# Kernel optimization log

Measured on AMD Instinct MI355X. Metric: run time of the kernel, lower is better.

Reference implementation:

```python
import jax, jax.numpy as jnp
import numpy as np

EPS = 1e-10  # faithful to original: masked scores are set to eps, not -inf


def setup_inputs() -> dict:
    key = jax.random.key(0)
    ks = jax.random.split(key, 5)
    B, S, D, N, H = 2, 2048, 1024, 16, 64
    init_range = 0.02
    residual = jax.random.normal(ks[0], (B, S, D), dtype=jnp.float32)
    W_key = jax.random.normal(ks[1], (N, D, H), dtype=jnp.float32) * init_range
    W_query = jax.random.normal(ks[2], (N, D, H), dtype=jnp.float32) * init_range
    W_values = jax.random.normal(ks[3], (N, D, H), dtype=jnp.float32) * init_range
    W_output = jax.random.normal(ks[4], (N, H, D), dtype=jnp.float32) * init_range
    return {
        "residual": residual,
        "W_key": W_key, "W_query": W_query, "W_values": W_values, "W_output": W_output,
        "Bias_key": jnp.zeros((N, H), jnp.float32),
        "Bias_query": jnp.zeros((N, H), jnp.float32),
        "Bias_values": jnp.zeros((N, H), jnp.float32),
        "Bias_output": jnp.zeros((D,), jnp.float32),
    }


def reference(residual, W_key, W_query, W_values, W_output,
              Bias_key, Bias_query, Bias_values, Bias_output):
    B, S, D = residual.shape
    N, _, H = W_key.shape
    # projections: [b,s,n,h]
    keys = jnp.einsum('bse,neh->bsnh', residual, W_key) + Bias_key
    queries = jnp.einsum('bse,neh->bsnh', residual, W_query) + Bias_query
    values = jnp.einsum('bse,neh->bsnh', residual, W_values) + Bias_values
    # scores: [b,n,q,k]
    scores = jnp.einsum('bknh,bqnh->bnqk', keys, queries) / jnp.sqrt(jnp.asarray(H, scores_dtype(residual)))
    q_idx = jnp.arange(S)[:, None]
    k_idx = jnp.arange(S)[None, :]
    causal_mask = q_idx < k_idx  # future positions
    # QUIRK of original module: masked scores are assigned eps (~0), not -inf
    scores = jnp.where(causal_mask[None, None, :, :], jnp.asarray(EPS, scores.dtype), scores)
    probs = jax.nn.softmax(scores, axis=3)
    weighted = jnp.einsum('bnqk,bknh->bqnh', probs, values)
    out = jnp.einsum('bqnh,nhe->bqe', weighted, W_output) + Bias_output
    return out


def scores_dtype(x):
    return x.dtype
```

## Files before the change

kernel.cpp:

```cpp
#include <hip/hip_runtime.h>
#include <hip/hip_bf16.h>
#include <cmath>

typedef __bf16 bf16;
typedef __attribute__((ext_vector_type(4))) __bf16 bf16x4;
typedef __attribute__((ext_vector_type(8))) __bf16 bf16x8;
typedef __attribute__((ext_vector_type(4))) float f32x4;

#define B_ 2
#define S_ 2048
#define D_ 1024
#define N_ 16
#define H_ 64
#define LOG2E 1.44269504088896340736f

__device__ __forceinline__ void gload16(const bf16* g, bf16* l) {
  __builtin_amdgcn_global_load_lds(
      (const __attribute__((address_space(1))) void*)(g),
      (__attribute__((address_space(3))) void*)(l), 16, 0, 0);
}

__device__ __forceinline__ f32x4 mfma16(bf16x8 a, bf16x8 b, f32x4 c) {
  return __builtin_amdgcn_mfma_f32_16x16x32_bf16(a, b, c, 0, 0, 0);
}

__device__ __forceinline__ f32x4 zero4() {
  f32x4 v = {0.0f, 0.0f, 0.0f, 0.0f};
  return v;
}

__global__ __launch_bounds__(256) void cvt_kernel(
    const float* __restrict__ in, bf16* __restrict__ out, int n8) {
  int id = blockIdx.x * 256 + threadIdx.x;
  if (id >= n8) return;
  const float4* p = (const float4*)(in + (size_t)id * 8);
  float4 v0 = p[0], v1 = p[1];
  bf16x8 o;
  o[0] = (bf16)v0.x; o[1] = (bf16)v0.y; o[2] = (bf16)v0.z; o[3] = (bf16)v0.w;
  o[4] = (bf16)v1.x; o[5] = (bf16)v1.y; o[6] = (bf16)v1.z; o[7] = (bf16)v1.w;
  *(bf16x8*)(out + (size_t)id * 8) = o;
}

__global__ __launch_bounds__(256) void qkvw_transpose_kernel(
    const float* __restrict__ Wk, const float* __restrict__ Wq,
    const float* __restrict__ Wv, bf16* __restrict__ out) {
  __shared__ bf16 t[64][72];
  const int z = blockIdx.z;
  const float* W = (z < 16) ? Wk : (z < 32) ? Wq : Wv;
  const float* ing = W + (size_t)(z & 15) * (1024 * 64);
  bf16* outg = out + (size_t)z * (64 * 1024);
  const int r0 = blockIdx.x * 64;
  const int t8 = threadIdx.x & 7, trow = threadIdx.x >> 3;
#pragma unroll
  for (int p = 0; p < 2; ++p) {
    int r = trow + p * 32;
    const float4* src = (const float4*)(ing + (size_t)(r0 + r) * 64 + t8 * 8);
    float4 v0 = src[0], v1 = src[1];
    bf16x8 o;
    o[0] = (bf16)v0.x; o[1] = (bf16)v0.y; o[2] = (bf16)v0.z; o[3] = (bf16)v0.w;
    o[4] = (bf16)v1.x; o[5] = (bf16)v1.y; o[6] = (bf16)v1.z; o[7] = (bf16)v1.w;
    *(bf16x8*)(&t[r][t8 * 8]) = o;
  }
  __syncthreads();
#pragma unroll
  for (int p = 0; p < 2; ++p) {
    int c = trow + p * 32;
    bf16x8 v;
#pragma unroll
    for (int j = 0; j < 8; ++j) v[j] = t[t8 * 8 + j][c];
    *(bf16x8*)(outg + (size_t)c * 1024 + r0 + t8 * 8) = v;
  }
}

__global__ __launch_bounds__(256) void transpose_f32bf16_kernel(
    const float* __restrict__ in, bf16* __restrict__ out, int R, int C) {
  __shared__ bf16 t[64][72];
  const size_t mat = (size_t)R * C;
  const float* ing = in + (size_t)blockIdx.z * mat;
  bf16* outg = out + (size_t)blockIdx.z * mat;
  const int r0 = blockIdx.x * 64, c0 = blockIdx.y * 64;
  const int t8 = threadIdx.x & 7, trow = threadIdx.x >> 3;
#pragma unroll
  for (int p = 0; p < 2; ++p) {
    int r = trow + p * 32;
    const float4* src = (const float4*)(ing + (size_t)(r0 + r) * C + c0 + t8 * 8);
    float4 v0 = src[0], v1 = src[1];
    bf16x8 o;
    o[0] = (bf16)v0.x; o[1] = (bf16)v0.y; o[2] = (bf16)v0.z; o[3] = (bf16)v0.w;
    o[4] = (bf16)v1.x; o[5] = (bf16)v1.y; o[6] = (bf16)v1.z; o[7] = (bf16)v1.w;
    *(bf16x8*)(&t[r][t8 * 8]) = o;
  }
  __syncthreads();
#pragma unroll
  for (int p = 0; p < 2; ++p) {
    int c = trow + p * 32;
    bf16x8 v;
#pragma unroll
    for (int j = 0; j < 8; ++j) v[j] = t[t8 * 8 + j][c];
    *(bf16x8*)(outg + (size_t)(c0 + c) * R + r0 + t8 * 8) = v;
  }
}

__global__ __launch_bounds__(256) void transpose_bf16_kernel(
    const bf16* __restrict__ in, bf16* __restrict__ out, int R, int C) {
  __shared__ bf16 t[64][72];
  const size_t mat = (size_t)R * C;
  const bf16* ing = in + (size_t)blockIdx.z * mat;
  bf16* outg = out + (size_t)blockIdx.z * mat;
  const int r0 = blockIdx.x * 64, c0 = blockIdx.y * 64;
  const int t8 = threadIdx.x & 7, trow = threadIdx.x >> 3;
#pragma unroll
  for (int p = 0; p < 2; ++p) {
    int r = trow + p * 32;
    bf16x8 v = *(const bf16x8*)(ing + (size_t)(r0 + r) * C + c0 + t8 * 8);
    *(bf16x8*)(&t[r][t8 * 8]) = v;
  }
  __syncthreads();
#pragma unroll
  for (int p = 0; p < 2; ++p) {
    int c = trow + p * 32;
    bf16x8 v;
#pragma unroll
    for (int j = 0; j < 8; ++j) v[j] = t[t8 * 8 + j][c];
    *(bf16x8*)(outg + (size_t)(c0 + c) * R + r0 + t8 * 8) = v;
  }
}

__global__ __launch_bounds__(256) void sufv_tot_kernel(
    const bf16* __restrict__ Vp, float* __restrict__ tot) {
  __shared__ float red[4][64];
  const int hd = blockIdx.x, seg = blockIdx.y;
  const int h = threadIdx.x & 63, sub = threadIdx.x >> 6;
  const bf16* Vh = Vp + (size_t)hd * S_ * H_;
  float a = 0.0f;
  const int k0 = seg * 32 + sub * 8;
#pragma unroll
  for (int k = 0; k < 8; ++k) a += (float)Vh[(size_t)(k0 + k) * H_ + h];
  red[sub][h] = a;
  __syncthreads();
  if (sub == 0)
    tot[(hd * 64 + seg) * 64 + h] = red[0][h] + red[1][h] + red[2][h] + red[3][h];
}

__global__ __launch_bounds__(64) void sufv_scan_kernel(
    bf16* __restrict__ VS, const float* __restrict__ tot) {
  const int hd = blockIdx.x, seg = blockIdx.y, h = threadIdx.x;
  bf16* Vh = VS + (size_t)hd * S_ * H_;
  float a = 0.0f;
  for (int s2 = seg + 1; s2 < 64; ++s2) a += tot[(hd * 64 + s2) * 64 + h];
  for (int k = seg * 32 + 31; k >= seg * 32; --k) {
    const float v = (float)Vh[(size_t)k * H_ + h];
    Vh[(size_t)k * H_ + h] = (bf16)a;
    a += v;
  }
}

__global__ __launch_bounds__(256) void gemm_proj_kernel(
    const bf16* __restrict__ A, const bf16* __restrict__ Bt,
    const float* __restrict__ bk, const float* __restrict__ bq,
    const float* __restrict__ bv, bf16* __restrict__ proj_base) {
  __shared__ bf16 As[128 * 64];
  __shared__ bf16 Bs[128 * 64];
  const int tid = threadIdx.x;
  const int w = tid >> 6, l = tid & 63, lan = l & 15, grp = l >> 4;
  const int mb = (w >> 1) * 64, nb = (w & 1) * 64;
  const int m0 = blockIdx.y * 128, n0 = blockIdx.x * 128;
  const int zc = n0 >> 10;
  const float* bias = (zc == 0) ? bk : (zc == 1 ? bq : bv);
  bf16* Out = proj_base + (size_t)zc * ((size_t)B_ * N_ * S_ * H_);
  const int lrow8 = l >> 3;
  const int swl = ((l & 7) ^ lrow8) * 8;
  const int l7 = lan & 7;

  f32x4 acc[4][4];
#pragma unroll
  for (int i = 0; i < 4; ++i)
#pragma unroll
    for (int j = 0; j < 4; ++j) acc[i][j] = zero4();

  for (int kb = 0; kb < 1024; kb += 64) {
    __syncthreads();
#pragma unroll
    for (int i = 0; i < 4; ++i) {
      int ch = w * 4 + i;
      gload16(A + (size_t)(m0 + ch * 8 + lrow8) * 1024 + kb + swl, As + ch * 512);
      gload16(Bt + (size_t)(n0 + ch * 8 + lrow8) * 1024 + kb + swl, Bs + ch * 512);
    }
    __syncthreads();
#pragma unroll
    for (int kk = 0; kk < 2; ++kk) {
      bf16x8 a[4], b[4];
#pragma unroll
      for (int mf = 0; mf < 4; ++mf)
        a[mf] = *(const bf16x8*)(As + (mb + mf * 16 + lan) * 64 + (((grp + kk * 4) ^ l7) << 3));
#pragma unroll
      for (int nf = 0; nf < 4; ++nf)
        b[nf] = *(const bf16x8*)(Bs + (nb + nf * 16 + lan) * 64 + (((grp + kk * 4) ^ l7) << 3));
#pragma unroll
      for (int mf = 0; mf < 4; ++mf)
#pragma unroll
        for (int nf = 0; nf < 4; ++nf)
          acc[mf][nf] = mfma16(a[mf], b[nf], acc[mf][nf]);
    }
  }
#pragma unroll
  for (int nf = 0; nf < 4; ++nf) {
    int c10 = (n0 + nb + nf * 16 + lan) & 1023;
    float bs = bias[c10];
    int n = c10 >> 6, h = c10 & 63;
#pragma unroll
    for (int mf = 0; mf < 4; ++mf) {
#pragma unroll
      for (int r = 0; r < 4; ++r) {
        int m = m0 + mb + mf * 16 + grp * 4 + r;
        int b = m >> 11, s = m & 2047;
        Out[((size_t)((b * N_ + n) * S_ + s)) * H_ + h] = (bf16)(acc[mf][nf][r] + bs);
      }
    }
  }
}

__global__ __launch_bounds__(256) void gemm_out_kernel(
    const bf16* __restrict__ A, const bf16* __restrict__ Bt,
    const float* __restrict__ bias, float* __restrict__ Out) {
  __shared__ bf16 As[128 * 64];
  __shared__ bf16 Bs[128 * 64];
  const int tid = threadIdx.x;
  const int w = tid >> 6, l = tid & 63, lan = l & 15, grp = l >> 4;
  const int mb = (w >> 1) * 64, nb = (w & 1) * 64;
  const int m0 = blockIdx.y * 128, n0 = blockIdx.x * 128;
  const int lrow8 = l >> 3;
  const int swl = ((l & 7) ^ lrow8) * 8;
  const int l7 = lan & 7;

  f32x4 acc[4][4];
#pragma unroll
  for (int i = 0; i < 4; ++i)
#pragma unroll
    for (int j = 0; j < 4; ++j) acc[i][j] = zero4();

  for (int kb = 0; kb < 1024; kb += 64) {
    __syncthreads();
#pragma unroll
    for (int i = 0; i < 4; ++i) {
      int ch = w * 4 + i;
      gload16(A + (size_t)(m0 + ch * 8 + lrow8) * 1024 + kb + swl, As + ch * 512);
      gload16(Bt + (size_t)(n0 + ch * 8 + lrow8) * 1024 + kb + swl, Bs + ch * 512);
    }
    __syncthreads();
#pragma unroll
    for (int kk = 0; kk < 2; ++kk) {
      bf16x8 a[4], b[4];
#pragma unroll
      for (int mf = 0; mf < 4; ++mf)
        a[mf] = *(const bf16x8*)(As + (mb + mf * 16 + lan) * 64 + (((grp + kk * 4) ^ l7) << 3));
#pragma unroll
      for (int nf = 0; nf < 4; ++nf)
        b[nf] = *(const bf16x8*)(Bs + (nb + nf * 16 + lan) * 64 + (((grp + kk * 4) ^ l7) << 3));
#pragma unroll
      for (int mf = 0; mf < 4; ++mf)
#pragma unroll
        for (int nf = 0; nf < 4; ++nf)
          acc[mf][nf] = mfma16(a[mf], b[nf], acc[mf][nf]);
    }
  }
#pragma unroll
  for (int nf = 0; nf < 4; ++nf) {
    int c = n0 + nb + nf * 16 + lan;
    float bs = bias[c];
#pragma unroll
    for (int mf = 0; mf < 4; ++mf) {
#pragma unroll
      for (int r = 0; r < 4; ++r) {
        int m = m0 + mb + mf * 16 + grp * 4 + r;
        Out[(size_t)m * 1024 + c] = acc[mf][nf][r] + bs;
      }
    }
  }
}

__global__ __launch_bounds__(256) void attn_kernel(
    const bf16* __restrict__ Qp, const bf16* __restrict__ Kp,
    const bf16* __restrict__ Vt, const bf16* __restrict__ Suf,
    bf16* __restrict__ Wtd, float* __restrict__ PoA, float* __restrict__ PoB,
    float* __restrict__ PpA, float* __restrict__ PpB) {
  __shared__ bf16 Ks[2][64 * 64];
  __shared__ bf16 Vs[2][64 * 64];
  __shared__ bf16 Ps[4][32 * 72];
  const int tid = threadIdx.x;
  const int w = tid >> 6, l = tid & 63, lan = l & 15, grp = l >> 4;
  const int bi = blockIdx.x;
  const int qq = bi >> 8;
  const int j = bi & 255;
  const int hd = j & 31, wv = j >> 5;
  int x, t0, t1;
  if (qq == 0)      { x = 15 - wv; t0 = 0;     t1 = x + 1; }
  else if (qq == 1) { x = 15 - wv; t0 = x + 1; t1 = 2 * x + 2; }
  else              { x = wv;      t0 = 0;     t1 = 2 * x + 2; }
  const int qw = x * 128 + w * 32;
  const bf16* Qh = Qp + (size_t)hd * S_ * H_;
  const bf16* Kh = Kp + (size_t)hd * S_ * H_;
  const bf16* Vh = Vt + (size_t)hd * H_ * S_;
  const bf16* Sufh = Suf + (size_t)hd * S_ * H_;
  const int lrow8 = l >> 3;
  const int swl = ((l & 7) ^ lrow8) * 8;
  const int l7 = lan & 7;
  const float cexp = 0.125f * LOG2E;

#define STAGE(buf, kb_)                                                        \
  do {                                                                         \
    _Pragma("unroll") for (int i2 = 0; i2 < 2; ++i2) {                         \
      int ch = w * 2 + i2;                                                     \
      gload16(Kh + (size_t)((kb_) + ch * 8 + lrow8) * H_ + swl,                \
              &Ks[buf][ch * 512]);                                             \
      gload16(Vh + (size_t)(ch * 8 + lrow8) * S_ + (kb_) + swl,                \
              &Vs[buf][ch * 512]);                                             \
    }                                                                          \
  } while (0)

  bf16x8 qa[2][2];
#pragma unroll
  for (int qt = 0; qt < 2; ++qt)
#pragma unroll
    for (int kf = 0; kf < 2; ++kf)
      qa[qt][kf] = *(const bf16x8*)(Qh + (size_t)(qw + qt * 16 + lan) * H_ + grp * 8 + kf * 32);

  f32x4 o[2][4];
  float psum[2] = {0.0f, 0.0f};
#pragma unroll
  for (int qt = 0; qt < 2; ++qt)
#pragma unroll
    for (int hf = 0; hf < 4; ++hf) o[qt][hf] = zero4();

  bf16* Pw = &Ps[w][0];

  STAGE(0, t0 * 64);
  for (int tt = t0; tt < t1; ++tt) {
    const int kb = tt * 64;
    const int cur = (tt - t0) & 1;
    if (tt + 1 < t1) {
      STAGE(cur ^ 1, kb + 64);
      asm volatile("s_waitcnt vmcnt(4)" ::: "memory");
    } else {
      asm volatile("s_waitcnt vmcnt(0)" ::: "memory");
    }
    __builtin_amdgcn_s_barrier();

    if (kb <= qw + 31) {
      const bf16* Kc = &Ks[cur][0];
      const bf16* Vc = &Vs[cur][0];

      f32x4 s2[4][2];
#pragma unroll
      for (int k2 = 0; k2 < 4; ++k2)
#pragma unroll
        for (int qt = 0; qt < 2; ++qt) s2[k2][qt] = zero4();
      __builtin_amdgcn_s_setprio(1);
#pragma unroll
      for (int kf = 0; kf < 2; ++kf) {
        bf16x8 kfr[4];
#pragma unroll
        for (int k2 = 0; k2 < 4; ++k2)
          kfr[k2] = *(const bf16x8*)(Kc + (k2 * 16 + lan) * 64 + (((grp + kf * 4) ^ l7) << 3));
#pragma unroll
        for (int k2 = 0; k2 < 4; ++k2)
#pragma unroll
          for (int qt = 0; qt < 2; ++qt)
            s2[k2][qt] = mfma16(kfr[k2], qa[qt][kf], s2[k2][qt]);
      }
      __builtin_amdgcn_s_setprio(0);

      const bool maskt = (kb + 63 > qw);
#pragma unroll
      for (int qt = 0; qt < 2; ++qt) {
        const int q_g = qw + qt * 16 + lan;
#pragma unroll
        for (int k2 = 0; k2 < 4; ++k2) {
          f32x4 p;
#pragma unroll
          for (int r = 0; r < 4; ++r) p[r] = exp2f(s2[k2][qt][r] * cexp);
          if (maskt) {
            const int kg0 = kb + k2 * 16 + grp * 4;
#pragma unroll
            for (int r = 0; r < 4; ++r)
              if (kg0 + r > q_g) p[r] = 0.0f;
          }
          psum[qt] += (p[0] + p[1]) + (p[2] + p[3]);
          unsigned plo, phi;
          asm("v_cvt_pk_bf16_f32 %0, %1, %2" : "=v"(plo) : "v"(p[0]), "v"(p[1]));
          asm("v_cvt_pk_bf16_f32 %0, %1, %2" : "=v"(phi) : "v"(p[2]), "v"(p[3]));
          uint2 u; u.x = plo; u.y = phi;
          *(uint2*)(Pw + (qt * 16 + lan) * 72 + k2 * 16 + grp * 4) = u;
        }
      }

      __builtin_amdgcn_s_setprio(1);
#pragma unroll
      for (int ks = 0; ks < 2; ++ks) {
        bf16x8 pa[2], vb[4];
#pragma unroll
        for (int qt = 0; qt < 2; ++qt)
          pa[qt] = *(const bf16x8*)(Pw + (qt * 16 + lan) * 72 + grp * 8 + ks * 32);
#pragma unroll
        for (int hf = 0; hf < 4; ++hf)
          vb[hf] = *(const bf16x8*)(Vc + (hf * 16 + lan) * 64 + (((grp + ks * 4) ^ l7) << 3));
#pragma unroll
        for (int qt = 0; qt < 2; ++qt)
#pragma unroll
          for (int hf = 0; hf < 4; ++hf)
            o[qt][hf] = mfma16(pa[qt], vb[hf], o[qt][hf]);
      }
      __builtin_amdgcn_s_setprio(0);
    }
    __builtin_amdgcn_s_barrier();
  }
#undef STAGE

#pragma unroll
  for (int qt = 0; qt < 2; ++qt) {
    psum[qt] += __shfl_xor(psum[qt], 16);
    psum[qt] += __shfl_xor(psum[qt], 32);
  }

  if (qq == 2) {
    const size_t outbase = (size_t)(hd >> 4) * S_ * (N_ * H_) + (size_t)(hd & 15) * H_;
#pragma unroll
    for (int qt = 0; qt < 2; ++qt) {
#pragma unroll
      for (int r = 0; r < 4; ++r) {
        const int q_g = qw + qt * 16 + grp * 4 + r;
        const float ps = __shfl(psum[qt], grp * 4 + r);
        const float inv = 1.0f / (ps + (float)(2047 - q_g));
#pragma unroll
        for (int hf = 0; hf < 4; ++hf) {
          const int h = hf * 16 + lan;
          const float suf = (float)Sufh[(size_t)q_g * H_ + h];
          Wtd[outbase + (size_t)q_g * (N_ * H_) + h] = (bf16)((o[qt][hf][r] + suf) * inv);
        }
      }
    }
  } else {
    float* Po = (qq == 0) ? PoA : PoB;
    float* Pp = (qq == 0) ? PpA : PpB;
    const int pb = (hd * 8 + (x - 8)) * 128 + w * 32;
#pragma unroll
    for (int qt = 0; qt < 2; ++qt) {
#pragma unroll
      for (int r = 0; r < 4; ++r) {
        const int rl = qt * 16 + grp * 4 + r;
        const float ps = __shfl(psum[qt], grp * 4 + r);
        if (lan == 0) Pp[pb + rl] = ps;
#pragma unroll
        for (int hf = 0; hf < 4; ++hf)
          Po[(size_t)(pb + rl) * 64 + hf * 16 + lan] = o[qt][hf][r];
      }
    }
  }
}

__global__ __launch_bounds__(256) void combine_kernel(
    const float* __restrict__ PoA, const float* __restrict__ PoB,
    const float* __restrict__ PpA, const float* __restrict__ PpB,
    const bf16* __restrict__ Suf, bf16* __restrict__ Wtd) {
  const int hd = blockIdx.x >> 3, xi = blockIdx.x & 7;
  const int x = xi + 8;
  const int pb = (hd * 8 + xi) * 128;
  const size_t outbase = (size_t)(hd >> 4) * S_ * (N_ * H_) + (size_t)(hd & 15) * H_;
#pragma unroll
  for (int it = 0; it < 8; ++it) {
    const int e = it * 256 + threadIdx.x;
    const int rl = e >> 4, h4 = (e & 15) * 4;
    const int q_g = x * 128 + rl;
    const float Z = PpA[pb + rl] + PpB[pb + rl] + (float)(2047 - q_g);
    const float inv = 1.0f / Z;
    const float4 a = *(const float4*)(PoA + (size_t)(pb + rl) * 64 + h4);
    const float4 b = *(const float4*)(PoB + (size_t)(pb + rl) * 64 + h4);
    const bf16x4 s4 = *(const bf16x4*)(Suf + ((size_t)hd * S_ + q_g) * 64 + h4);
    bf16x4 ov;
    ov[0] = (bf16)((a.x + b.x + (float)s4[0]) * inv);
    ov[1] = (bf16)((a.y + b.y + (float)s4[1]) * inv);
    ov[2] = (bf16)((a.z + b.z + (float)s4[2]) * inv);
    ov[3] = (bf16)((a.w + b.w + (float)s4[3]) * inv);
    *(bf16x4*)(Wtd + outbase + (size_t)q_g * (N_ * H_) + h4) = ov;
  }
}

extern "C" void kernel_launch(void* const* d_in, const int* in_sizes, int n_in,
                              void* d_out, int out_size, void* d_ws, size_t ws_size,
                              hipStream_t stream) {
  const float* residual = (const float*)d_in[0];
  const float* Wk = (const float*)d_in[1];
  const float* Wq = (const float*)d_in[2];
  const float* Wv = (const float*)d_in[3];
  const float* Wo = (const float*)d_in[4];
  const float* Bk = (const float*)d_in[5];
  const float* Bq = (const float*)d_in[6];
  const float* Bv = (const float*)d_in[7];
  const float* Bo = (const float*)d_in[8];
  float* outp = (float*)d_out;

  char* ws = (char*)d_ws;
  const size_t MB = 1024 * 1024;
  bf16* Abf = (bf16*)(ws + 0 * MB);
  bf16* Wot = (bf16*)(ws + 8 * MB);
  bf16* Wkt = (bf16*)(ws + 10 * MB);
  bf16* Kp  = (bf16*)(ws + 16 * MB);
  bf16* Qp  = (bf16*)(ws + 24 * MB);
  bf16* Vp  = (bf16*)(ws + 32 * MB);
  bf16* Vtp = (bf16*)(ws + 40 * MB);
  bf16* Wtd = Abf;
  float* PpA = (float*)(ws + 10 * MB);
  float* PpB = (float*)(ws + 10 * MB + 128 * 1024);
  float* tot = (float*)(ws + 10 * MB + 256 * 1024);
  bf16* Suf = Vp;
  float* PoA = (float*)d_out;
  float* PoB = (float*)d_out + 2 * 1024 * 1024;
  (void)in_sizes; (void)n_in; (void)out_size; (void)ws_size;

  cvt_kernel<<<2048, 256, 0, stream>>>(residual, Abf, (B_ * S_ * D_) / 8);

  qkvw_transpose_kernel<<<dim3(16, 1, 48), 256, 0, stream>>>(Wk, Wq, Wv, Wkt);
  transpose_f32bf16_kernel<<<dim3(16, 16, 1), 256, 0, stream>>>(Wo, Wot, 1024, 1024);

  gemm_proj_kernel<<<dim3(24, 32), 256, 0, stream>>>(Abf, Wkt, Bk, Bq, Bv, Kp);

  sufv_tot_kernel<<<dim3(32, 64), 256, 0, stream>>>(Vp, tot);
  transpose_bf16_kernel<<<dim3(32, 1, 32), 256, 0, stream>>>(Vp, Vtp, 2048, 64);
  sufv_scan_kernel<<<dim3(32, 64), 64, 0, stream>>>(Vp, tot);

  attn_kernel<<<768, 256, 0, stream>>>(Qp, Kp, Vtp, Suf, Wtd, PoA, PoB, PpA, PpB);

  combine_kernel<<<256, 256, 0, stream>>>(PoA, PoB, PpA, PpB, Suf, Wtd);

  gemm_out_kernel<<<dim3(8, 32, 1), 256, 0, stream>>>(Wtd, Wot, Bo, outp);
}
```

Baseline: 155.2 us.

## Rewrite QKV projection GEMM with 256x256 tiles and double-buffered LDS pipeline

The QKV projection GEMM moves from 128x128 tiles with 4 waves to 256x256 tiles with 8 waves, each wave computing a 128x64 sub-tile. It double-buffers LDS across K-halves and issues the global-to-LDS loads for the next K step in between MFMA phases, with explicit vmcnt waits and barriers. It also raises MFMA priority via s_setprio. The aim is to overlap memory latency with compute and raise arithmetic intensity, at the cost of more registers and LDS per block and only 192 blocks, which may underfill the GPU's CUs.

New measurement: 149.0 us. -4.0%, faster.

```diff
diff --git a/kernel.cpp b/kernel.cpp
--- a/kernel.cpp
+++ b/kernel.cpp
@@ -155,66 +155,112 @@
   }
 }
 
-__global__ __launch_bounds__(256) void gemm_proj_kernel(
+__global__ __launch_bounds__(512) void gemm_proj_kernel(
     const bf16* __restrict__ A, const bf16* __restrict__ Bt,
     const float* __restrict__ bk, const float* __restrict__ bq,
     const float* __restrict__ bv, bf16* __restrict__ proj_base) {
-  __shared__ bf16 As[128 * 64];
-  __shared__ bf16 Bs[128 * 64];
+  __shared__ bf16 As[2][2][256 * 32];
+  __shared__ bf16 Bs[2][2][256 * 32];
   const int tid = threadIdx.x;
   const int w = tid >> 6, l = tid & 63, lan = l & 15, grp = l >> 4;
-  const int mb = (w >> 1) * 64, nb = (w & 1) * 64;
-  const int m0 = blockIdx.y * 128, n0 = blockIdx.x * 128;
+  const int wm128 = (w >> 2) * 128, wn64 = (w & 3) * 64;
+  const int m0 = blockIdx.y * 256, n0 = blockIdx.x * 256;
   const int zc = n0 >> 10;
   const float* bias = (zc == 0) ? bk : (zc == 1 ? bq : bv);
   bf16* Out = proj_base + (size_t)zc * ((size_t)B_ * N_ * S_ * H_);
-  const int lrow8 = l >> 3;
-  const int swl = ((l & 7) ^ lrow8) * 8;
-  const int l7 = lan & 7;
-
-  f32x4 acc[4][4];
-#pragma unroll
-  for (int i = 0; i < 4; ++i)
-#pragma unroll
-    for (int j = 0; j < 4; ++j) acc[i][j] = zero4();
-
-  for (int kb = 0; kb < 1024; kb += 64) {
-    __syncthreads();
-#pragma unroll
-    for (int i = 0; i < 4; ++i) {
-      int ch = w * 4 + i;
-      gload16(A + (size_t)(m0 + ch * 8 + lrow8) * 1024 + kb + swl, As + ch * 512);
-      gload16(Bt + (size_t)(n0 + ch * 8 + lrow8) * 1024 + kb + swl, Bs + ch * 512);
-    }
-    __syncthreads();
-#pragma unroll
-    for (int kk = 0; kk < 2; ++kk) {
-      bf16x8 a[4], b[4];
-#pragma unroll
-      for (int mf = 0; mf < 4; ++mf)
-        a[mf] = *(const bf16x8*)(As + (mb + mf * 16 + lan) * 64 + (((grp + kk * 4) ^ l7) << 3));
-#pragma unroll
-      for (int nf = 0; nf < 4; ++nf)
-        b[nf] = *(const bf16x8*)(Bs + (nb + nf * 16 + lan) * 64 + (((grp + kk * 4) ^ l7) << 3));
-#pragma unroll
-      for (int mf = 0; mf < 4; ++mf)
-#pragma unroll
-        for (int nf = 0; nf < 4; ++nf)
-          acc[mf][nf] = mfma16(a[mf], b[nf], acc[mf][nf]);
-    }
-  }
+  const int posx = (grp ^ ((lan >> 1) & 3)) << 3;
+
+#define STG(LDS_, GP_, rb_, buf_, kh_, kb_)                                    \
+  do {                                                                         \
+    _Pragma("unroll") for (int jj = 0; jj < 2; ++jj) {                         \
+      const int ci = jj * 512 + tid;                                           \
+      const int rw = ci >> 2, cp = ci & 3;                                     \
+      const int gg = cp ^ ((rw >> 1) & 3);                                     \
+      gload16(GP_ + (size_t)((rb_) + rw) * 1024 + (kb_) + (kh_) * 32 + gg * 8, \
+              &LDS_[buf_][kh_][(jj * 512 + w * 64) * 8]);                      \
+    }                                                                          \
+  } while (0)
+
+  f32x4 acc[8][4];
+#pragma unroll
+  for (int i = 0; i < 8; ++i)
+#pragma unroll
+    for (int jv = 0; jv < 4; ++jv) acc[i][jv] = zero4();
+
+  bf16x8 b[4];
+
+#define DO_PHASE(buf_, mq_, kk_, READB_)                                       \
+  do {                                                                         \
+    if (READB_) {                                                              \
+      _Pragma("unroll") for (int nf = 0; nf < 4; ++nf)                         \
+        b[nf] = *(const bf16x8*)(&Bs[buf_][kk_][(wn64 + nf * 16 + lan) * 32 + posx]); \
+    }                                                                          \
+    bf16x8 a[4];                                                               \
+    _Pragma("unroll") for (int mf = 0; mf < 4; ++mf)                           \
+      a[mf] = *(const bf16x8*)(&As[buf_][kk_][(wm128 + (mq_) * 64 + mf * 16 + lan) * 32 + posx]); \
+    __builtin_amdgcn_s_setprio(1);                                             \
+    _Pragma("unroll") for (int mf = 0; mf < 4; ++mf)                           \
+      _Pragma("unroll") for (int nf = 0; nf < 4; ++nf)                         \
+        acc[(mq_) * 4 + mf][nf] = mfma16(a[mf], b[nf], acc[(mq_) * 4 + mf][nf]); \
+    __builtin_amdgcn_s_setprio(0);                                             \
+  } while (0)
+
+  STG(As, A, m0, 0, 0, 0);
+  STG(Bs, Bt, n0, 0, 0, 0);
+  STG(As, A, m0, 0, 1, 0);
+  STG(Bs, Bt, n0, 0, 1, 0);
+
+  for (int t = 0; t < 15; ++t) {
+    const int buf = t & 1;
+    const int nkb = (t + 1) * 64;
+    STG(As, A, m0, buf ^ 1, 0, nkb);
+    asm volatile("s_waitcnt vmcnt(6)" ::: "memory");
+    __builtin_amdgcn_s_barrier();
+    asm volatile("" ::: "memory");
+    DO_PHASE(buf, 0, 0, true);
+    STG(Bs, Bt, n0, buf ^ 1, 0, nkb);
+    asm volatile("" ::: "memory");
+    __builtin_amdgcn_s_barrier();
+    asm volatile("" ::: "memory");
+    DO_PHASE(buf, 1, 0, false);
+    STG(As, A, m0, buf ^ 1, 1, nkb);
+    asm volatile("s_waitcnt vmcnt(6)" ::: "memory");
+    __builtin_amdgcn_s_barrier();
+    asm volatile("" ::: "memory");
+    DO_PHASE(buf, 0, 1, true);
+    STG(Bs, Bt, n0, buf ^ 1, 1, nkb);
+    asm volatile("" ::: "memory");
+    __builtin_amdgcn_s_barrier();
+    asm volatile("" ::: "memory");
+    DO_PHASE(buf, 1, 1, false);
+  }
+  {
+    asm volatile("s_waitcnt vmcnt(4)" ::: "memory");
+    __builtin_amdgcn_s_barrier();
+    asm volatile("" ::: "memory");
+    DO_PHASE(1, 0, 0, true);
+    DO_PHASE(1, 1, 0, false);
+    asm volatile("s_waitcnt vmcnt(0)" ::: "memory");
+    __builtin_amdgcn_s_barrier();
+    asm volatile("" ::: "memory");
+    DO_PHASE(1, 0, 1, true);
+    DO_PHASE(1, 1, 1, false);
+  }
+#undef STG
+#undef DO_PHASE
+
 #pragma unroll
   for (int nf = 0; nf < 4; ++nf) {
-    int c10 = (n0 + nb + nf * 16 + lan) & 1023;
-    float bs = bias[c10];
-    int n = c10 >> 6, h = c10 & 63;
-#pragma unroll
-    for (int mf = 0; mf < 4; ++mf) {
+    const int c10 = (n0 + wn64 + nf * 16 + lan) & 1023;
+    const float bs = bias[c10];
+    const int n = c10 >> 6, h = c10 & 63;
+#pragma unroll
+    for (int am = 0; am < 8; ++am) {
 #pragma unroll
       for (int r = 0; r < 4; ++r) {
-        int m = m0 + mb + mf * 16 + grp * 4 + r;
-        int b = m >> 11, s = m & 2047;
-        Out[((size_t)((b * N_ + n) * S_ + s)) * H_ + h] = (bf16)(acc[mf][nf][r] + bs);
+        const int m = m0 + wm128 + am * 16 + grp * 4 + r;
+        const int bb = m >> 11, s = m & 2047;
+        Out[((size_t)((bb * N_ + n) * S_ + s)) * H_ + h] = (bf16)(acc[am][nf][r] + bs);
       }
     }
   }
@@ -522,7 +568,7 @@
   qkvw_transpose_kernel<<<dim3(16, 1, 48), 256, 0, stream>>>(Wk, Wq, Wv, Wkt);
   transpose_f32bf16_kernel<<<dim3(16, 16, 1), 256, 0, stream>>>(Wo, Wot, 1024, 1024);
 
-  gemm_proj_kernel<<<dim3(24, 32), 256, 0, stream>>>(Abf, Wkt, Bk, Bq, Bv, Kp);
+  gemm_proj_kernel<<<dim3(12, 16), 512, 0, stream>>>(Abf, Wkt, Bk, Bq, Bv, Kp);
 
   sufv_tot_kernel<<<dim3(32, 64), 256, 0, stream>>>(Vp, tot);
   transpose_bf16_kernel<<<dim3(32, 1, 32), 256, 0, stream>>>(Vp, Vtp, 2048, 64);
```
